# Kernel tuning notes

Measured on AMD Instinct MI355X. Metric: run time of the kernel, lower is better.

## Reference

```python
import jax, jax.numpy as jnp
import numpy as np

N_NODES = 100000
N_EDGES = 3200000


def gcn_conv(x, W, b, row, col, n):
    # PyG GCNConv: add self-loops, symmetric normalization D^-1/2 (A+I) D^-1/2 (X W) + b
    xw = x @ W  # [N, out]
    loops = jnp.arange(n)
    row2 = jnp.concatenate([row, loops])
    col2 = jnp.concatenate([col, loops])
    deg = jax.ops.segment_sum(jnp.ones_like(col2, dtype=xw.dtype), col2, num_segments=n)
    dinv = jnp.where(deg > 0, jax.lax.rsqrt(deg), 0.0)
    norm = dinv[row2] * dinv[col2]  # [E+N]
    msg = xw[row2] * norm[:, None]  # gather + scale
    out = jax.ops.segment_sum(msg, col2, num_segments=n)  # scatter-add to targets
    return out + b


def setup_inputs() -> dict:
    key = jax.random.key(0)
    ks = jax.random.split(key, 9)
    x = jax.random.normal(ks[0], (N_NODES, 2), dtype=jnp.float32)
    edge_index = jax.random.randint(ks[1], (2, N_EDGES), 0, N_NODES, dtype=jnp.int64)
    edge_attr = jax.random.normal(ks[2], (N_EDGES, 1), dtype=jnp.float32)
    # params (glorot-ish scale)
    W1 = jax.random.normal(ks[3], (2, 16), dtype=jnp.float32) * (1.0 / np.sqrt(2))
    b1 = jnp.zeros((16,), dtype=jnp.float32)
    We = jax.random.normal(ks[4], (33, 4), dtype=jnp.float32) * (1.0 / np.sqrt(33))
    be = jnp.zeros((4,), dtype=jnp.float32)
    W2 = jax.random.normal(ks[5], (16, 2), dtype=jnp.float32) * (1.0 / np.sqrt(16))
    b2 = jnp.zeros((2,), dtype=jnp.float32)
    return {"x": x, "edge_index": edge_index, "edge_attr": edge_attr,
            "W1": W1, "b1": b1, "We": We, "be": be, "W2": W2, "b2": b2}


def reference(x, edge_index, edge_attr, W1, b1, We, be, W2, b2):
    row, col = edge_index[0], edge_index[1]
    n = x.shape[0]
    h = gcn_conv(x, W1, b1, row, col, n)  # [N, 16]
    # edge update: gather src/dst features, concat with edge_attr, Linear+ReLU
    e_in = jnp.concatenate([h[row], edge_attr, h[col]], axis=1)  # [E, 33]
    e_out = jax.nn.relu(e_in @ We + be)  # [E, 4]
    out_x = gcn_conv(h, W2, b2, row, col, n)  # [N, 2]
    return jax.nn.log_softmax(out_x, axis=1), jax.nn.log_softmax(e_out, axis=1)
```

## Files before the change

### kernel.cpp

```cpp
#include <hip/hip_runtime.h>


#define BLK 256
#define BLKN 1024
#define BLKP 1024
#define CH 12500
#define VIT ((CH + 4 * BLKP - 1) / (4 * BLKP))
#define BSH 7
#define BSZ 128
#define NBMAX 1024
#define PAD 16
#define CAP 8192
#define CAPSH 13
#define S1 262144.0f
#define S2 65536.0f
#define BIAS 8388608

__global__ __launch_bounds__(BLKP) void k_part(const int* __restrict__ row,
                                               const int* __restrict__ col,
                                               int* __restrict__ gcursor,
                                               unsigned* __restrict__ part,
                                               int E, int NB) {
    __shared__ int hist[NBMAX];
    __shared__ int lstart[NBMAX];
    __shared__ int lcur[NBMAX];
    __shared__ int gb[NBMAX];
    __shared__ unsigned sbuf[CH];
    __shared__ unsigned short bid[CH];
    __shared__ int wsum[BLKP / 64];
    int t = threadIdx.x;
    int e0 = blockIdx.x * CH;
    int cnt = min(CH, E - e0);
    if (t < NBMAX) hist[t] = 0;
    __syncthreads();
    int4 cv[VIT];
    #pragma unroll
    for (int i = 0; i < VIT; i++) {
        int k = 4 * (t + i * BLKP);
        if (k + 3 < cnt) {
            int4 c = *reinterpret_cast<const int4*>(col + e0 + k);
            cv[i] = c;
            atomicAdd(&hist[c.x >> BSH], 1);
            atomicAdd(&hist[c.y >> BSH], 1);
            atomicAdd(&hist[c.z >> BSH], 1);
            atomicAdd(&hist[c.w >> BSH], 1);
        } else if (k < cnt) {
            int4 c = make_int4(0, 0, 0, 0);
            int m = cnt - k;
            c.x = col[e0 + k];             atomicAdd(&hist[c.x >> BSH], 1);
            if (m > 1) { c.y = col[e0 + k + 1]; atomicAdd(&hist[c.y >> BSH], 1); }
            if (m > 2) { c.z = col[e0 + k + 2]; atomicAdd(&hist[c.z >> BSH], 1); }
            cv[i] = c;
        }
    }
    __syncthreads();
    int h = hist[t];
    int lane = t & 63, wid = t >> 6;
    int v = h;
    #pragma unroll
    for (int off = 1; off < 64; off <<= 1) {
        int u = __shfl_up(v, off);
        if (lane >= off) v += u;
    }
    if (lane == 63) wsum[wid] = v;
    __syncthreads();
    int base = v - h;
    for (int w = 0; w < wid; w++) base += wsum[w];
    lstart[t] = base;
    lcur[t]   = base;
    gb[t] = (t << CAPSH) + (h ? atomicAdd(&gcursor[t * PAD], h) : 0);
    __syncthreads();
    #pragma unroll
    for (int i = 0; i < VIT; i++) {
        int k = 4 * (t + i * BLKP);
        if (k + 3 < cnt) {
            int4 r = *reinterpret_cast<const int4*>(row + e0 + k);
            int4 c = cv[i];
            int b0 = c.x >> BSH, b1 = c.y >> BSH, b2 = c.z >> BSH, b3 = c.w >> BSH;
            int o0 = atomicAdd(&lcur[b0], 1);
            int o1 = atomicAdd(&lcur[b1], 1);
            int o2 = atomicAdd(&lcur[b2], 1);
            int o3 = atomicAdd(&lcur[b3], 1);
            sbuf[o0] = ((unsigned)r.x << BSH) | (unsigned)(c.x & (BSZ - 1));
            sbuf[o1] = ((unsigned)r.y << BSH) | (unsigned)(c.y & (BSZ - 1));
            sbuf[o2] = ((unsigned)r.z << BSH) | (unsigned)(c.z & (BSZ - 1));
            sbuf[o3] = ((unsigned)r.w << BSH) | (unsigned)(c.w & (BSZ - 1));
            bid[o0] = (unsigned short)b0;
            bid[o1] = (unsigned short)b1;
            bid[o2] = (unsigned short)b2;
            bid[o3] = (unsigned short)b3;
        } else if (k < cnt) {
            int m = cnt - k;
            int cs[3] = {cv[i].x, cv[i].y, cv[i].z};
            for (int q = 0; q < m && q < 3; q++) {
                int c = cs[q];
                int r = row[e0 + k + q];
                int b = c >> BSH;
                int off = atomicAdd(&lcur[b], 1);
                sbuf[off] = ((unsigned)r << BSH) | (unsigned)(c & (BSZ - 1));
                bid[off] = (unsigned short)b;
            }
        }
    }
    __syncthreads();
    for (int j = t; j < cnt; j += BLKP) {
        int b = bid[j];
        part[gb[b] + (j - lstart[b])] = sbuf[j];
    }
}

__global__ __launch_bounds__(BLKN) void k_nodeA(const unsigned* __restrict__ part,
                        const int* __restrict__ gcursor,
                        const float2* __restrict__ x2, float* __restrict__ dinv,
                        int* __restrict__ degi, int2* __restrict__ pi, int N) {
    __shared__ int cnt[BSZ];
    int t = threadIdx.x;
    if (t < BSZ) cnt[t] = 0;
    __syncthreads();
    int b = blockIdx.x;
    int j0 = b << CAPSH, j1 = j0 + gcursor[b * PAD];
    for (int j = j0 + 4 * t; j < j1; j += 4 * BLKN) {
        int m = j1 - j;
        if (m >= 4) {
            unsigned w0 = part[j], w1 = part[j + 1], w2 = part[j + 2], w3 = part[j + 3];
            atomicAdd(&cnt[w0 & (BSZ - 1)], 1);
            atomicAdd(&cnt[w1 & (BSZ - 1)], 1);
            atomicAdd(&cnt[w2 & (BSZ - 1)], 1);
            atomicAdd(&cnt[w3 & (BSZ - 1)], 1);
        } else {
            for (int q = 0; q < m; q++)
                atomicAdd(&cnt[part[j + q] & (BSZ - 1)], 1);
        }
    }
    __syncthreads();
    if (t < BSZ) {
        int node = (b << BSH) + t;
        if (node < N) {
            int dg = cnt[t];
            degi[node] = dg;
            float d = rsqrtf((float)(dg + 1));
            dinv[node] = d;
            float2 xv = x2[node];
            pi[node] = make_int2(__float2int_rn(xv.x * d * S1),
                                 __float2int_rn(xv.y * d * S1));
        }
    }
}

__device__ __forceinline__ unsigned long long packi2(int2 p) {
    return ((unsigned long long)(unsigned)p.x << 32) | (unsigned)(p.y + BIAS);
}

__global__ __launch_bounds__(BLKN) void k_nodeB(const unsigned* __restrict__ part,
                        const int* __restrict__ gcursor,
                        const float* __restrict__ dinv, const int* __restrict__ degi,
                        const int2* __restrict__ pi,
                        const float* __restrict__ W1, const float* __restrict__ b1,
                        const float* __restrict__ W2, const float* __restrict__ We,
                        const float* __restrict__ be,
                        float4* __restrict__ U, float4* __restrict__ V,
                        int2* __restrict__ qi, int N) {
    __shared__ unsigned long long acc[BSZ];
    __shared__ float sW1[32], sb1[16], sW2[32], sWr[64], sWc[64], sbe[4];
    int t = threadIdx.x;
    if (t < BSZ) acc[t] = 0ull;
    if (t < 32) sW1[t] = W1[t];
    else if (t < 64) sW2[t - 32] = W2[t - 32];
    else if (t < 80) sb1[t - 64] = b1[t - 64];
    else if (t < 144) sWr[t - 80] = We[t - 80];
    else if (t < 208) sWc[t - 144] = We[68 + (t - 144)];
    else if (t < 212) sbe[t - 208] = be[t - 208];
    __syncthreads();
    int b = blockIdx.x;
    int j0 = b << CAPSH, j1 = j0 + gcursor[b * PAD];
    for (int j = j0 + 4 * t; j < j1; j += 4 * BLKN) {
        int m = j1 - j;
        if (m >= 4) {
            unsigned w0 = part[j], w1 = part[j + 1], w2 = part[j + 2], w3 = part[j + 3];
            int2 p0 = pi[w0 >> BSH], p1 = pi[w1 >> BSH];
            int2 p2 = pi[w2 >> BSH], p3 = pi[w3 >> BSH];
            atomicAdd(&acc[w0 & (BSZ - 1)], packi2(p0));
            atomicAdd(&acc[w1 & (BSZ - 1)], packi2(p1));
            atomicAdd(&acc[w2 & (BSZ - 1)], packi2(p2));
            atomicAdd(&acc[w3 & (BSZ - 1)], packi2(p3));
        } else {
            for (int q = 0; q < m; q++) {
                unsigned w = part[j + q];
                atomicAdd(&acc[w & (BSZ - 1)], packi2(pi[w >> BSH]));
            }
        }
    }
    __syncthreads();
    if (t < BSZ) {
        int node = (b << BSH) + t;
        if (node < N) {
            unsigned long long a = acc[t];
            int sx = (int)(unsigned)(a >> 32);
            long long sy = (long long)(unsigned)(a & 0xffffffffull)
                         - (long long)degi[node] * BIAS;
            int2 ps = pi[node];
            float d = dinv[node];
            float ax = (float)(ps.x + (long long)sx) * (1.0f / S1);
            float ay = (float)(ps.y + sy) * (1.0f / S1);
            float s0 = d * ax, s1 = d * ay;
            float u0 = sbe[0], u1 = sbe[1], u2 = sbe[2], u3 = sbe[3];
            float v0 = 0.f, v1 = 0.f, v2 = 0.f, v3 = 0.f;
            float w0 = 0.f, w1 = 0.f;
            #pragma unroll
            for (int jj = 0; jj < 16; jj++) {
                float hj = fmaf(s0, sW1[jj], fmaf(s1, sW1[16 + jj], sb1[jj]));
                u0 = fmaf(hj, sWr[4 * jj + 0], u0);
                u1 = fmaf(hj, sWr[4 * jj + 1], u1);
                u2 = fmaf(hj, sWr[4 * jj + 2], u2);
                u3 = fmaf(hj, sWr[4 * jj + 3], u3);
                v0 = fmaf(hj, sWc[4 * jj + 0], v0);
                v1 = fmaf(hj, sWc[4 * jj + 1], v1);
                v2 = fmaf(hj, sWc[4 * jj + 2], v2);
                v3 = fmaf(hj, sWc[4 * jj + 3], v3);
                w0 = fmaf(hj, sW2[2 * jj], w0);
                w1 = fmaf(hj, sW2[2 * jj + 1], w1);
            }
            U[node] = make_float4(u0, u1, u2, u3);
            V[node] = make_float4(v0, v1, v2, v3);
            float qx = w0 * d, qy = w1 * d;
            qi[node] = make_int2(__float2int_rn(qx * S2), __float2int_rn(qy * S2));
        }
    }
}

__device__ __forceinline__ float4 edge_lsm(float4 u, float4 v, float av,
                                           const float* sW16) {
    float a0 = u.x + fmaf(av, sW16[0], v.x);
    float a1 = u.y + fmaf(av, sW16[1], v.y);
    float a2 = u.z + fmaf(av, sW16[2], v.z);
    float a3 = u.w + fmaf(av, sW16[3], v.w);
    a0 = fmaxf(a0, 0.f); a1 = fmaxf(a1, 0.f);
    a2 = fmaxf(a2, 0.f); a3 = fmaxf(a3, 0.f);
    float m = fmaxf(fmaxf(a0, a1), fmaxf(a2, a3));
    float s = expf(a0 - m) + expf(a1 - m) + expf(a2 - m) + expf(a3 - m);
    float l = m + logf(s);
    return make_float4(a0 - l, a1 - l, a2 - l, a3 - l);
}

__global__ void k_tail(const int* __restrict__ row, const int* __restrict__ col,
                       const float* __restrict__ ea, const float4* __restrict__ U,
                       const float4* __restrict__ V, const float* __restrict__ We,
                       float4* __restrict__ eout,
                       const unsigned* __restrict__ part, const int* __restrict__ gcursor,
                       const float* __restrict__ dinv, const int* __restrict__ degi,
                       const int2* __restrict__ qi, const float* __restrict__ b2,
                       float2* __restrict__ outn, int E, int N, int EB) {
    __shared__ unsigned long long acc[BSZ];
    int t = threadIdx.x;
    if (blockIdx.x < (unsigned)EB) {
        float* sW16 = (float*)acc;
        if (t < 4) sW16[t] = We[64 + t];
        __syncthreads();
        int base = blockIdx.x * (4 * BLK);
        int e0 = base + t;
        if (base + 4 * BLK <= E) {
            int r0 = row[e0], r1 = row[e0 + BLK], r2 = row[e0 + 2 * BLK], r3 = row[e0 + 3 * BLK];
            int c0 = col[e0], c1 = col[e0 + BLK], c2 = col[e0 + 2 * BLK], c3 = col[e0 + 3 * BLK];
            float a0 = ea[e0], a1 = ea[e0 + BLK], a2 = ea[e0 + 2 * BLK], a3 = ea[e0 + 3 * BLK];
            float4 u0 = U[r0], u1 = U[r1], u2 = U[r2], u3 = U[r3];
            float4 v0 = V[c0], v1 = V[c1], v2 = V[c2], v3 = V[c3];
            eout[e0]           = edge_lsm(u0, v0, a0, sW16);
            eout[e0 + BLK]     = edge_lsm(u1, v1, a1, sW16);
            eout[e0 + 2 * BLK] = edge_lsm(u2, v2, a2, sW16);
            eout[e0 + 3 * BLK] = edge_lsm(u3, v3, a3, sW16);
        } else {
            for (int q = 0; q < 4; q++) {
                int e = e0 + q * BLK;
                if (e < E)
                    eout[e] = edge_lsm(U[row[e]], V[col[e]], ea[e], sW16);
            }
        }
        return;
    }
    int b = blockIdx.x - EB;
    if (t < BSZ) acc[t] = 0ull;
    __syncthreads();
    int j0 = b << CAPSH, j1 = j0 + gcursor[b * PAD];
    for (int j = j0 + 4 * t; j < j1; j += 4 * BLK) {
        int m = j1 - j;
        if (m >= 4) {
            unsigned w0 = part[j], w1 = part[j + 1], w2 = part[j + 2], w3 = part[j + 3];
            int2 q0 = qi[w0 >> BSH], q1 = qi[w1 >> BSH];
            int2 q2 = qi[w2 >> BSH], q3 = qi[w3 >> BSH];
            atomicAdd(&acc[w0 & (BSZ - 1)], packi2(q0));
            atomicAdd(&acc[w1 & (BSZ - 1)], packi2(q1));
            atomicAdd(&acc[w2 & (BSZ - 1)], packi2(q2));
            atomicAdd(&acc[w3 & (BSZ - 1)], packi2(q3));
        } else {
            for (int q = 0; q < m; q++) {
                unsigned w = part[j + q];
                atomicAdd(&acc[w & (BSZ - 1)], packi2(qi[w >> BSH]));
            }
        }
    }
    __syncthreads();
    if (t < BSZ) {
        int node = (b << BSH) + t;
        if (node < N) {
            unsigned long long a = acc[t];
            int sx = (int)(unsigned)(a >> 32);
            long long sy = (long long)(unsigned)(a & 0xffffffffull)
                         - (long long)degi[node] * BIAS;
            int2 qs = qi[node];
            float d = dinv[node];
            float bx = (float)(qs.x + (long long)sx) * (1.0f / S2);
            float by = (float)(qs.y + sy) * (1.0f / S2);
            float o0 = fmaf(d, bx, b2[0]);
            float o1 = fmaf(d, by, b2[1]);
            float m = fmaxf(o0, o1);
            float l2 = m + logf(expf(o0 - m) + expf(o1 - m));
            outn[node] = make_float2(o0 - l2, o1 - l2);
        }
    }
}

extern "C" void kernel_launch(void* const* d_in, const int* in_sizes, int n_in,
                              void* d_out, int out_size, void* d_ws, size_t ws_size,
                              hipStream_t stream) {
    const float* x  = (const float*)d_in[0];
    const int*   ei = (const int*)d_in[1];
    const float* ea = (const float*)d_in[2];
    const float* W1 = (const float*)d_in[3];
    const float* b1 = (const float*)d_in[4];
    const float* We = (const float*)d_in[5];
    const float* be = (const float*)d_in[6];
    const float* W2 = (const float*)d_in[7];
    const float* b2 = (const float*)d_in[8];

    const int N = in_sizes[0] / 2;
    const int E = in_sizes[2];
    const int* row = ei;
    const int* col = ei + E;
    const int NB  = (N + BSZ - 1) >> BSH;
    const int NCH = (E + CH - 1) / CH;
    const int EB  = (E + 4 * BLK - 1) / (4 * BLK);

    float2* out_nodes = (float2*)d_out;
    float4* out_edges = (float4*)((float*)d_out + 2 * (size_t)N);

    char* ws = (char*)d_ws;
    int*      gcursor = (int*)     (ws + 0);
    float*    dinv    = (float*)   (ws + 65536);
    int*      degi    = (int*)     (ws + 465536);
    int2*     pi      = (int2*)    (ws + 865536);
    int2*     qi      = (int2*)    (ws + 1665536);
    float4*   U       = (float4*)  (ws + 2465536);
    float4*   V       = (float4*)  (ws + 4065536);
    unsigned* part    = (unsigned*)(ws + 5665536);

    hipMemsetAsync(gcursor, 0, NBMAX * PAD * sizeof(int), stream);
    k_part <<<NCH, BLKP, 0, stream>>>(row, col, gcursor, part, E, NB);
    k_nodeA<<<NB,  BLKN, 0, stream>>>(part, gcursor, (const float2*)x, dinv, degi, pi, N);
    k_nodeB<<<NB,  BLKN, 0, stream>>>(part, gcursor, dinv, degi, pi, W1, b1, W2, We, be, U, V, qi, N);
    k_tail <<<EB + NB, BLK, 0, stream>>>(row, col, ea, U, V, We, out_edges,
                                         part, gcursor, dinv, degi, qi, b2,
                                         out_nodes, E, N, EB);
}
```

Measured before the change: 208.3 us.

## Fuse node degree and aggregation kernels with grid barrier and LDS-cached partition

Merges the degree-count kernel and the first aggregation kernel into one launch. Each block stages its bucket's edge list in shared memory once and reuses it for both passes. A global atomic spin barrier separates the degree phase from the aggregation phase, and the per-node degree comes from shared counts instead of global arrays. The tail kernel now puts node blocks first so they start early. The grid barrier assumes all 782 blocks of 256 threads (about 40KB LDS each) are co-resident. The barrier counter sits inside the memset region so it is reset each call.

```diff
diff --git a/kernel.cpp b/kernel.cpp
--- a/kernel.cpp
+++ b/kernel.cpp
@@ -2,7 +2,6 @@
 
 
 #define BLK 256
-#define BLKN 1024
 #define BLKP 1024
 #define CH 12500
 #define VIT ((CH + 4 * BLKP - 1) / (4 * BLKP))
@@ -109,29 +108,47 @@
     }
 }
 
-__global__ __launch_bounds__(BLKN) void k_nodeA(const unsigned* __restrict__ part,
+__device__ __forceinline__ unsigned long long packi2(int2 p) {
+    return ((unsigned long long)(unsigned)p.x << 32) | (unsigned)(p.y + BIAS);
+}
+
+__global__ __launch_bounds__(BLK) void k_nodeAB(const unsigned* __restrict__ part,
                         const int* __restrict__ gcursor,
-                        const float2* __restrict__ x2, float* __restrict__ dinv,
-                        int* __restrict__ degi, int2* __restrict__ pi, int N) {
+                        const float2* __restrict__ x2,
+                        float* __restrict__ dinv, int* __restrict__ degi,
+                        int2* __restrict__ pi,
+                        const float* __restrict__ W1, const float* __restrict__ b1,
+                        const float* __restrict__ W2, const float* __restrict__ We,
+                        const float* __restrict__ be,
+                        float4* __restrict__ U, float4* __restrict__ V,
+                        int2* __restrict__ qi, int* __restrict__ bar,
+                        int N, int NB) {
+    __shared__ unsigned sbuf[CAP];
+    __shared__ unsigned long long acc[BSZ];
     __shared__ int cnt[BSZ];
+    __shared__ float sW1[32], sb1[16], sW2[32], sWr[64], sWc[64], sbe[4];
     int t = threadIdx.x;
-    if (t < BSZ) cnt[t] = 0;
-    __syncthreads();
     int b = blockIdx.x;
-    int j0 = b << CAPSH, j1 = j0 + gcursor[b * PAD];
-    for (int j = j0 + 4 * t; j < j1; j += 4 * BLKN) {
-        int m = j1 - j;
-        if (m >= 4) {
-            unsigned w0 = part[j], w1 = part[j + 1], w2 = part[j + 2], w3 = part[j + 3];
-            atomicAdd(&cnt[w0 & (BSZ - 1)], 1);
-            atomicAdd(&cnt[w1 & (BSZ - 1)], 1);
-            atomicAdd(&cnt[w2 & (BSZ - 1)], 1);
-            atomicAdd(&cnt[w3 & (BSZ - 1)], 1);
-        } else {
-            for (int q = 0; q < m; q++)
-                atomicAdd(&cnt[part[j + q] & (BSZ - 1)], 1);
-        }
-    }
+    int n = gcursor[b * PAD];
+    int j0 = b << CAPSH;
+    if (t < BSZ) { cnt[t] = 0; acc[t] = 0ull; }
+    if (t < 32) sW1[t] = W1[t];
+    else if (t < 64) sW2[t - 32] = W2[t - 32];
+    else if (t < 80) sb1[t - 64] = b1[t - 64];
+    else if (t < 144) sWr[t - 80] = We[t - 80];
+    else if (t < 208) sWc[t - 144] = We[68 + (t - 144)];
+    else if (t < 212) sbe[t - 208] = be[t - 208];
+    __syncthreads();
+    for (int j = 4 * t; j + 3 < n; j += 4 * BLK)
+        *reinterpret_cast<int4*>(&sbuf[j]) =
+            *reinterpret_cast<const int4*>(part + j0 + j);
+    {
+        int jt = (n & ~3) + t;
+        if (jt < n) sbuf[jt] = part[j0 + jt];
+    }
+    __syncthreads();
+    for (int j = t; j < n; j += BLK)
+        atomicAdd(&cnt[sbuf[j] & (BSZ - 1)], 1);
     __syncthreads();
     if (t < BSZ) {
         int node = (b << BSH) + t;
@@ -145,38 +162,16 @@
                                  __float2int_rn(xv.y * d * S1));
         }
     }
-}
-
-__device__ __forceinline__ unsigned long long packi2(int2 p) {
-    return ((unsigned long long)(unsigned)p.x << 32) | (unsigned)(p.y + BIAS);
-}
-
-__global__ __launch_bounds__(BLKN) void k_nodeB(const unsigned* __restrict__ part,
-                        const int* __restrict__ gcursor,
-                        const float* __restrict__ dinv, const int* __restrict__ degi,
-                        const int2* __restrict__ pi,
-                        const float* __restrict__ W1, const float* __restrict__ b1,
-                        const float* __restrict__ W2, const float* __restrict__ We,
-                        const float* __restrict__ be,
-                        float4* __restrict__ U, float4* __restrict__ V,
-                        int2* __restrict__ qi, int N) {
-    __shared__ unsigned long long acc[BSZ];
-    __shared__ float sW1[32], sb1[16], sW2[32], sWr[64], sWc[64], sbe[4];
-    int t = threadIdx.x;
-    if (t < BSZ) acc[t] = 0ull;
-    if (t < 32) sW1[t] = W1[t];
-    else if (t < 64) sW2[t - 32] = W2[t - 32];
-    else if (t < 80) sb1[t - 64] = b1[t - 64];
-    else if (t < 144) sWr[t - 80] = We[t - 80];
-    else if (t < 208) sWc[t - 144] = We[68 + (t - 144)];
-    else if (t < 212) sbe[t - 208] = be[t - 208];
-    __syncthreads();
-    int b = blockIdx.x;
-    int j0 = b << CAPSH, j1 = j0 + gcursor[b * PAD];
-    for (int j = j0 + 4 * t; j < j1; j += 4 * BLKN) {
-        int m = j1 - j;
+    __syncthreads();
+    if (t == 0) {
+        __hip_atomic_fetch_add(bar, 1, __ATOMIC_ACQ_REL, __HIP_MEMORY_SCOPE_AGENT);
+        while (__hip_atomic_load(bar, __ATOMIC_ACQUIRE, __HIP_MEMORY_SCOPE_AGENT) < NB) {}
+    }
+    __syncthreads();
+    for (int j = 4 * t; j < n; j += 4 * BLK) {
+        int m = n - j;
         if (m >= 4) {
-            unsigned w0 = part[j], w1 = part[j + 1], w2 = part[j + 2], w3 = part[j + 3];
+            unsigned w0 = sbuf[j], w1 = sbuf[j + 1], w2 = sbuf[j + 2], w3 = sbuf[j + 3];
             int2 p0 = pi[w0 >> BSH], p1 = pi[w1 >> BSH];
             int2 p2 = pi[w2 >> BSH], p3 = pi[w3 >> BSH];
             atomicAdd(&acc[w0 & (BSZ - 1)], packi2(p0));
@@ -185,7 +180,7 @@
             atomicAdd(&acc[w3 & (BSZ - 1)], packi2(p3));
         } else {
             for (int q = 0; q < m; q++) {
-                unsigned w = part[j + q];
+                unsigned w = sbuf[j + q];
                 atomicAdd(&acc[w & (BSZ - 1)], packi2(pi[w >> BSH]));
             }
         }
@@ -197,9 +192,9 @@
             unsigned long long a = acc[t];
             int sx = (int)(unsigned)(a >> 32);
             long long sy = (long long)(unsigned)(a & 0xffffffffull)
-                         - (long long)degi[node] * BIAS;
+                         - (long long)cnt[t] * BIAS;
             int2 ps = pi[node];
-            float d = dinv[node];
+            float d = rsqrtf((float)(cnt[t] + 1));
             float ax = (float)(ps.x + (long long)sx) * (1.0f / S1);
             float ay = (float)(ps.y + sy) * (1.0f / S1);
             float s0 = d * ax, s1 = d * ay;
@@ -249,14 +244,14 @@
                        const unsigned* __restrict__ part, const int* __restrict__ gcursor,
                        const float* __restrict__ dinv, const int* __restrict__ degi,
                        const int2* __restrict__ qi, const float* __restrict__ b2,
-                       float2* __restrict__ outn, int E, int N, int EB) {
+                       float2* __restrict__ outn, int E, int N, int NB) {
     __shared__ unsigned long long acc[BSZ];
     int t = threadIdx.x;
-    if (blockIdx.x < (unsigned)EB) {
+    if (blockIdx.x >= (unsigned)NB) {
         float* sW16 = (float*)acc;
         if (t < 4) sW16[t] = We[64 + t];
         __syncthreads();
-        int base = blockIdx.x * (4 * BLK);
+        int base = (blockIdx.x - NB) * (4 * BLK);
         int e0 = base + t;
         if (base + 4 * BLK <= E) {
             int r0 = row[e0], r1 = row[e0 + BLK], r2 = row[e0 + 2 * BLK], r3 = row[e0 + 3 * BLK];
@@ -277,7 +272,7 @@
         }
         return;
     }
-    int b = blockIdx.x - EB;
+    int b = blockIdx.x;
     if (t < BSZ) acc[t] = 0ull;
     __syncthreads();
     int j0 = b << CAPSH, j1 = j0 + gcursor[b * PAD];
@@ -345,6 +340,7 @@
 
     char* ws = (char*)d_ws;
     int*      gcursor = (int*)     (ws + 0);
+    int*      bar     = gcursor + 16000;
     float*    dinv    = (float*)   (ws + 65536);
     int*      degi    = (int*)     (ws + 465536);
     int2*     pi      = (int2*)    (ws + 865536);
@@ -354,10 +350,10 @@
     unsigned* part    = (unsigned*)(ws + 5665536);
 
     hipMemsetAsync(gcursor, 0, NBMAX * PAD * sizeof(int), stream);
-    k_part <<<NCH, BLKP, 0, stream>>>(row, col, gcursor, part, E, NB);
-    k_nodeA<<<NB,  BLKN, 0, stream>>>(part, gcursor, (const float2*)x, dinv, degi, pi, N);
-    k_nodeB<<<NB,  BLKN, 0, stream>>>(part, gcursor, dinv, degi, pi, W1, b1, W2, We, be, U, V, qi, N);
-    k_tail <<<EB + NB, BLK, 0, stream>>>(row, col, ea, U, V, We, out_edges,
-                                         part, gcursor, dinv, degi, qi, b2,
-                                         out_nodes, E, N, EB);
-}
+    k_part  <<<NCH, BLKP, 0, stream>>>(row, col, gcursor, part, E, NB);
+    k_nodeAB<<<NB,  BLK,  0, stream>>>(part, gcursor, (const float2*)x, dinv, degi,
+                                       pi, W1, b1, W2, We, be, U, V, qi, bar, N, NB);
+    k_tail  <<<NB + EB, BLK, 0, stream>>>(row, col, ea, U, V, We, out_edges,
+                                          part, gcursor, dinv, degi, qi, b2,
+                                          out_nodes, E, N, NB);
+}
```

Result: slower. 246.7 us (+18.4%).
